# Performance work log

Hardware: AMD Instinct MI355X
Metric: run time of the kernel (lower is better)

## Reference

```python
import jax, jax.numpy as jnp
import numpy as np

B, N, D, H = 2, 2048, 1024, 16
DH = D // H  # head dim = 64


def setup_inputs() -> dict:
    key = jax.random.key(0)
    ks = jax.random.split(key, 5)
    s = 0.02  # small init so softmax is well-behaved
    x = jax.random.normal(ks[0], (B, N, D), dtype=jnp.float32)
    mask = jnp.tril(jnp.ones((N, N), dtype=jnp.int32))[None, None]  # [1,1,N,N] causal
    Wq = jax.random.normal(ks[1], (D, D), dtype=jnp.float32) * s
    Wk = jax.random.normal(ks[2], (D, D), dtype=jnp.float32) * s
    Wv = jax.random.normal(ks[3], (D, D), dtype=jnp.float32) * s
    Wp = jax.random.normal(ks[4], (D, D), dtype=jnp.float32) * s
    zb = jnp.zeros((D,), dtype=jnp.float32)
    return {"x": x, "mask": mask, "Wq": Wq, "bq": zb, "Wk": Wk, "bk": zb,
            "Wv": Wv, "bv": zb, "Wp": Wp, "bp": zb}


def reference(x, mask, Wq, bq, Wk, bk, Wv, bv, Wp, bp):
    b, n, d = x.shape
    dh = d // H
    scale = 1.0 / np.sqrt(dh).astype(np.float32)

    def split_heads(t):  # [B,N,D] -> [B,H,N,dh]
        return t.reshape(b, n, H, dh).transpose(0, 2, 1, 3)

    q = split_heads(x @ Wq + bq)
    k = split_heads(x @ Wk + bk)
    v = split_heads(x @ Wv + bv)

    scores = jnp.einsum("bhqd,bhkd->bhqk", q, k) * scale  # [B,H,N,N]
    scores = jnp.where(mask[:, :, :n, :n] == 0, -jnp.inf, scores)
    A = jax.nn.softmax(scores, axis=-1)
    # dropout layers are identity at eval / pdrop=0
    y = jnp.einsum("bhqk,bhkd->bhqd", A, v)  # [B,H,N,dh]
    y = y.transpose(0, 2, 1, 3).reshape(b, n, d)
    y = y @ Wp + bp
    return (y, A)
```

## Files before the change

kernel.cpp:

```cpp
#include <hip/hip_runtime.h>
#include <hip/hip_bf16.h>
#include <math.h>

#define B_  2
#define N_  2048
#define D_  1024
#define H_  16
#define DH_ 64
#define QT  64
#define NQT (N_/QT)

typedef __attribute__((ext_vector_type(8))) short bf16x8;
typedef __attribute__((ext_vector_type(4))) float f32x4;

#define ASYNC16(g, l) __builtin_amdgcn_global_load_lds( \
    (const __attribute__((address_space(1))) void*)(g), \
    (__attribute__((address_space(3))) void*)(l), 16, 0, 0)

__device__ __forceinline__ short f2bf(float f) {
    __hip_bfloat16 h = __float2bfloat16(f);
    return *(short*)&h;
}

__global__ __launch_bounds__(256) void cast_kernel(
    const float* __restrict__ in, short* __restrict__ out)
{
    const int i = (blockIdx.x * 256 + threadIdx.x) * 8;
    float4 a = *(const float4*)(in + i);
    float4 b = *(const float4*)(in + i + 4);
    bf16x8 o;
    o[0] = f2bf(a.x); o[1] = f2bf(a.y); o[2] = f2bf(a.z); o[3] = f2bf(a.w);
    o[4] = f2bf(b.x); o[5] = f2bf(b.y); o[6] = f2bf(b.z); o[7] = f2bf(b.w);
    *(bf16x8*)(out + i) = o;
}

__global__ __launch_bounds__(256) void tc_kernel(
    const float* __restrict__ in, short* __restrict__ out, int K, int Nc)
{
    __shared__ float t[64][65];
    const int tid = threadIdx.x;
    const int k0 = blockIdx.y * 64, n0 = blockIdx.x * 64;
    #pragma unroll
    for (int p = 0; p < 4; ++p) {
        const int r = p * 16 + (tid >> 4);
        const int c = (tid & 15) * 4;
        float4 v = *(const float4*)(in + (size_t)(k0 + r) * Nc + n0 + c);
        t[r][c] = v.x; t[r][c+1] = v.y; t[r][c+2] = v.z; t[r][c+3] = v.w;
    }
    __syncthreads();
    #pragma unroll
    for (int p = 0; p < 4; ++p) {
        const int n = p * 16 + (tid >> 4);
        const int c = (tid & 15) * 4;
        ushort4 o;
        o.x = (unsigned short)f2bf(t[c + 0][n]);
        o.y = (unsigned short)f2bf(t[c + 1][n]);
        o.z = (unsigned short)f2bf(t[c + 2][n]);
        o.w = (unsigned short)f2bf(t[c + 3][n]);
        *(ushort4*)(out + (size_t)(n0 + n) * K + k0 + c) = o;
    }
}

__global__ __launch_bounds__(256) void gemm_mfma(
    const short* __restrict__ A, const short* __restrict__ Bt,
    const float* __restrict__ bias, void* __restrict__ outv,
    int M, int Nc, int K, int mode)
{
    __shared__ short As[128 * 64];
    __shared__ short Bs[128 * 64];

    const int tid  = threadIdx.x;
    const int w    = tid >> 6;
    const int lane = tid & 63;
    const int quad = lane >> 4;
    const int col  = lane & 15;
    const int wr   = (w >> 1) * 64;
    const int wc   = (w & 1) * 64;

    const int rowBase = blockIdx.y * 128;
    const int colBase = blockIdx.x * 128;

    const int srow = tid >> 3;
    const int scol = (tid & 7) * 8;

    f32x4 acc[4][4];
    #pragma unroll
    for (int i = 0; i < 4; ++i)
        #pragma unroll
        for (int j = 0; j < 4; ++j) acc[i][j] = (f32x4){0.f, 0.f, 0.f, 0.f};

    for (int k0 = 0; k0 < K; k0 += 64) {
        __syncthreads();
        #pragma unroll
        for (int i = 0; i < 4; ++i) {
            ASYNC16(A + (size_t)(rowBase + i * 32 + srow) * K + k0 + scol,
                    As + i * 2048 + tid * 8);
            ASYNC16(Bt + (size_t)(colBase + i * 32 + srow) * K + k0 + scol,
                    Bs + i * 2048 + tid * 8);
        }
        __syncthreads();

        #pragma unroll
        for (int kk = 0; kk < 2; ++kk) {
            bf16x8 af[4], bf[4];
            #pragma unroll
            for (int mt = 0; mt < 4; ++mt)
                af[mt] = *(const bf16x8*)&As[(wr + mt * 16 + col) * 64 + kk * 32 + quad * 8];
            #pragma unroll
            for (int nt = 0; nt < 4; ++nt)
                bf[nt] = *(const bf16x8*)&Bs[(wc + nt * 16 + col) * 64 + kk * 32 + quad * 8];
            #pragma unroll
            for (int mt = 0; mt < 4; ++mt)
                #pragma unroll
                for (int nt = 0; nt < 4; ++nt)
                    acc[mt][nt] = __builtin_amdgcn_mfma_f32_16x16x32_bf16(
                        af[mt], bf[nt], acc[mt][nt], 0, 0, 0);
        }
    }

    #pragma unroll
    for (int mt = 0; mt < 4; ++mt) {
        #pragma unroll
        for (int r = 0; r < 4; ++r) {
            const int rr = rowBase + wr + mt * 16 + quad * 4 + r;
            #pragma unroll
            for (int nt = 0; nt < 4; ++nt) {
                const int cc = colBase + wc + nt * 16 + col;
                float v = acc[mt][nt][r] + bias[cc];
                if (mode == 1) {
                    ((float*)outv)[(size_t)rr * Nc + cc] = v;
                } else {
                    const int b  = rr >> 11;
                    const int n  = rr & (N_ - 1);
                    const int h  = cc >> 6;
                    const int dh = cc & 63;
                    short hv = f2bf(v);
                    if (mode == 0)
                        ((short*)outv)[(((size_t)(b * H_ + h)) * N_ + n) * DH_ + dh] = hv;
                    else
                        ((short*)outv)[(((size_t)(b * H_ + h)) * DH_ + dh) * N_ + n] = hv;
                }
            }
        }
    }
}

__global__ __launch_bounds__(256) void attn_mfma_kernel(
    const __hip_bfloat16* __restrict__ Qb, const __hip_bfloat16* __restrict__ Kb,
    const __hip_bfloat16* __restrict__ Vtb, float* __restrict__ Aout,
    short* __restrict__ Ypre)
{
    __shared__ short p_lds[4][16][72];

    const int tid  = threadIdx.x;
    const int w    = tid >> 6;
    const int lane = tid & 63;
    const int quad = lane >> 4;
    const int col  = lane & 15;

    const int bid = blockIdx.x;
    const int bh  = bid & 31;
    const int qt  = (NQT - 1) - (bid >> 5);
    const int qbase = qt * QT;
    const size_t kvbase = (size_t)bh * N_ * DH_;

    const short* Qs = (const short*)Qb + kvbase;
    const short* Ks = (const short*)Kb + kvbase;
    const short* Vs = (const short*)Vtb + kvbase;

    const short* qrow = Qs + (size_t)(qbase + w * 16 + col) * DH_ + quad * 8;
    const bf16x8 qf0 = *(const bf16x8*)(qrow);
    const bf16x8 qf1 = *(const bf16x8*)(qrow + 32);

    const int mrow_g = qbase + w * 16 + quad * 4;

    float mrun[4] = {-1e30f, -1e30f, -1e30f, -1e30f};
    float lrun[4] = {0.f, 0.f, 0.f, 0.f};

    const int njt = qt + 1;

    for (int jt = 0; jt < njt; ++jt) {
        const int jbase = jt * QT;
        f32x4 s[4];
        #pragma unroll
        for (int nt = 0; nt < 4; ++nt) {
            const short* krow = Ks + (size_t)(jbase + nt * 16 + col) * DH_ + quad * 8;
            bf16x8 k0 = *(const bf16x8*)(krow);
            bf16x8 k1 = *(const bf16x8*)(krow + 32);
            f32x4 c = {0.f, 0.f, 0.f, 0.f};
            c = __builtin_amdgcn_mfma_f32_16x16x32_bf16(qf0, k0, c, 0, 0, 0);
            c = __builtin_amdgcn_mfma_f32_16x16x32_bf16(qf1, k1, c, 0, 0, 0);
            s[nt] = c;
        }
        const bool diag = (jt == qt);
        #pragma unroll
        for (int nt = 0; nt < 4; ++nt) {
            const int n_g = jbase + nt * 16 + col;
            #pragma unroll
            for (int r = 0; r < 4; ++r) {
                float v = s[nt][r] * 0.125f;
                if (diag && (n_g > mrow_g + r)) v = -1e30f;
                s[nt][r] = v;
            }
        }
        #pragma unroll
        for (int r = 0; r < 4; ++r) {
            float tmax = fmaxf(fmaxf(s[0][r], s[1][r]), fmaxf(s[2][r], s[3][r]));
            #pragma unroll
            for (int off = 1; off < 16; off <<= 1)
                tmax = fmaxf(tmax, __shfl_xor(tmax, off));
            float mnew = fmaxf(mrun[r], tmax);
            float psum = __expf(s[0][r] - mnew) + __expf(s[1][r] - mnew)
                       + __expf(s[2][r] - mnew) + __expf(s[3][r] - mnew);
            #pragma unroll
            for (int off = 1; off < 16; off <<= 1)
                psum += __shfl_xor(psum, off);
            lrun[r] = lrun[r] * __expf(mrun[r] - mnew) + psum;
            mrun[r] = mnew;
        }
    }

    float invl[4];
    #pragma unroll
    for (int r = 0; r < 4; ++r) invl[r] = 1.0f / lrun[r];

    f32x4 yacc[4] = {{0.f,0.f,0.f,0.f},{0.f,0.f,0.f,0.f},{0.f,0.f,0.f,0.f},{0.f,0.f,0.f,0.f}};

    for (int jt = 0; jt < njt; ++jt) {
        const int jbase = jt * QT;
        f32x4 s[4];
        #pragma unroll
        for (int nt = 0; nt < 4; ++nt) {
            const short* krow = Ks + (size_t)(jbase + nt * 16 + col) * DH_ + quad * 8;
            bf16x8 k0 = *(const bf16x8*)(krow);
            bf16x8 k1 = *(const bf16x8*)(krow + 32);
            f32x4 c = {0.f, 0.f, 0.f, 0.f};
            c = __builtin_amdgcn_mfma_f32_16x16x32_bf16(qf0, k0, c, 0, 0, 0);
            c = __builtin_amdgcn_mfma_f32_16x16x32_bf16(qf1, k1, c, 0, 0, 0);
            s[nt] = c;
        }
        const bool diag = (jt == qt);
        #pragma unroll
        for (int nt = 0; nt < 4; ++nt) {
            const int n_g = jbase + nt * 16 + col;
            #pragma unroll
            for (int r = 0; r < 4; ++r) {
                float v = s[nt][r] * 0.125f;
                if (diag && (n_g > mrow_g + r)) v = -1e30f;
                float p = __expf(v - mrun[r]);
                Aout[((size_t)bh * N_ + (mrow_g + r)) * N_ + n_g] = p * invl[r];
                p_lds[w][quad * 4 + r][nt * 16 + col] = f2bf(p);
            }
        }
        bf16x8 pa0 = *(const bf16x8*)&p_lds[w][col][quad * 8];
        bf16x8 pa1 = *(const bf16x8*)&p_lds[w][col][32 + quad * 8];
        #pragma unroll
        for (int dt = 0; dt < 4; ++dt) {
            const short* vrow = Vs + (size_t)(dt * 16 + col) * N_ + jbase + quad * 8;
            bf16x8 v0 = *(const bf16x8*)(vrow);
            bf16x8 v1 = *(const bf16x8*)(vrow + 32);
            yacc[dt] = __builtin_amdgcn_mfma_f32_16x16x32_bf16(pa0, v0, yacc[dt], 0, 0, 0);
            yacc[dt] = __builtin_amdgcn_mfma_f32_16x16x32_bf16(pa1, v1, yacc[dt], 0, 0, 0);
        }
    }

    const int b = bh >> 4, h = bh & 15;
    #pragma unroll
    for (int dt = 0; dt < 4; ++dt)
        #pragma unroll
        for (int r = 0; r < 4; ++r)
            Ypre[((size_t)b * N_ + mrow_g + r) * D_ + h * DH_ + dt * 16 + col]
                = f2bf(yacc[dt][r] * invl[r]);

    float4 z; z.x = 0.f; z.y = 0.f; z.z = 0.f; z.w = 0.f;
    for (int r = 0; r < QT; ++r) {
        float4* row = (float4*)(Aout + ((size_t)bh * N_ + qbase + r) * N_);
        for (int c4 = (qt + 1) * (QT / 4) + tid; c4 < N_ / 4; c4 += 256)
            row[c4] = z;
    }
}

extern "C" void kernel_launch(void* const* d_in, const int* in_sizes, int n_in,
                              void* d_out, int out_size, void* d_ws, size_t ws_size,
                              hipStream_t stream) {
    const float* x  = (const float*)d_in[0];
    const float* Wq = (const float*)d_in[2];
    const float* bq = (const float*)d_in[3];
    const float* Wk = (const float*)d_in[4];
    const float* bk = (const float*)d_in[5];
    const float* Wv = (const float*)d_in[6];
    const float* bv = (const float*)d_in[7];
    const float* Wp = (const float*)d_in[8];
    const float* bp = (const float*)d_in[9];

    float* out_y = (float*)d_out;
    float* out_A = out_y + (size_t)B_ * N_ * D_;

    const size_t qkv = (size_t)B_ * H_ * N_ * DH_;
    const size_t wsz = (size_t)D_ * D_;
    short* Q    = (short*)d_ws;
    short* K    = Q + qkv;
    short* Vt   = K + qkv;
    short* xb   = Vt + qkv;
    short* Ypre = xb + qkv;
    short* Wqt  = Ypre + qkv;
    short* Wkt  = Wqt + wsz;
    short* Wvt  = Wkt + wsz;
    short* Wpt  = Wvt + wsz;

    const int M = B_ * N_;
    dim3 ggrid(D_ / 128, M / 128);
    dim3 tgrid(D_ / 64, D_ / 64);

    cast_kernel<<<(int)(qkv / (256 * 8)), 256, 0, stream>>>(x, xb);
    tc_kernel<<<tgrid, 256, 0, stream>>>(Wq, Wqt, D_, D_);
    tc_kernel<<<tgrid, 256, 0, stream>>>(Wk, Wkt, D_, D_);
    tc_kernel<<<tgrid, 256, 0, stream>>>(Wv, Wvt, D_, D_);
    tc_kernel<<<tgrid, 256, 0, stream>>>(Wp, Wpt, D_, D_);

    gemm_mfma<<<ggrid, 256, 0, stream>>>(xb, Wqt, bq, Q,  M, D_, D_, 0);
    gemm_mfma<<<ggrid, 256, 0, stream>>>(xb, Wkt, bk, K,  M, D_, D_, 0);
    gemm_mfma<<<ggrid, 256, 0, stream>>>(xb, Wvt, bv, Vt, M, D_, D_, 2);

    attn_mfma_kernel<<<NQT * B_ * H_, 256, 0, stream>>>(
        (const __hip_bfloat16*)Q, (const __hip_bfloat16*)K,
        (const __hip_bfloat16*)Vt, out_A, Ypre);

    gemm_mfma<<<ggrid, 256, 0, stream>>>(Ypre, Wpt, bp, out_y, M, D_, D_, 1);
}
```

Baseline: 867.3 us.

## Transpose attention score MFMA so each lane owns one query row

The attention kernel swaps the MFMA operand order so each lane holds one query row's scores across four consecutive keys. The per-row softmax statistics then need only two cross-quad shuffles instead of four-step butterflies per row, and the A matrix can be written with float4 stores instead of scattered scalar stores. The launcher also batches the four weight transposes into one grid and the three QKV projections into one GEMM launch, cutting launch count and idle tail. The row inverse-sum is staged through LDS for the Y epilogue, which relies on each warp writing and reading only its own slot.

```diff
diff --git a/kernel.cpp b/kernel.cpp
--- a/kernel.cpp
+++ b/kernel.cpp
@@ -34,17 +34,23 @@
     *(bf16x8*)(out + i) = o;
 }
 
-__global__ __launch_bounds__(256) void tc_kernel(
-    const float* __restrict__ in, short* __restrict__ out, int K, int Nc)
+__global__ __launch_bounds__(256) void tc4_kernel(
+    const float* __restrict__ Wq, const float* __restrict__ Wk,
+    const float* __restrict__ Wv, const float* __restrict__ Wp,
+    short* __restrict__ out_base)
 {
     __shared__ float t[64][65];
+    const int z = blockIdx.z;
+    const float* in = (z == 0) ? Wq : (z == 1) ? Wk : (z == 2) ? Wv : Wp;
+    short* out = out_base + (size_t)z * D_ * D_;
+
     const int tid = threadIdx.x;
     const int k0 = blockIdx.y * 64, n0 = blockIdx.x * 64;
     #pragma unroll
     for (int p = 0; p < 4; ++p) {
         const int r = p * 16 + (tid >> 4);
         const int c = (tid & 15) * 4;
-        float4 v = *(const float4*)(in + (size_t)(k0 + r) * Nc + n0 + c);
+        float4 v = *(const float4*)(in + (size_t)(k0 + r) * D_ + n0 + c);
         t[r][c] = v.x; t[r][c+1] = v.y; t[r][c+2] = v.z; t[r][c+3] = v.w;
     }
     __syncthreads();
@@ -57,18 +63,16 @@
         o.y = (unsigned short)f2bf(t[c + 1][n]);
         o.z = (unsigned short)f2bf(t[c + 2][n]);
         o.w = (unsigned short)f2bf(t[c + 3][n]);
-        *(ushort4*)(out + (size_t)(n0 + n) * K + k0 + c) = o;
-    }
-}
-
-__global__ __launch_bounds__(256) void gemm_mfma(
+        *(ushort4*)(out + (size_t)(n0 + n) * D_ + k0 + c) = o;
+    }
+}
+
+__device__ __forceinline__ void gemm_body(
     const short* __restrict__ A, const short* __restrict__ Bt,
     const float* __restrict__ bias, void* __restrict__ outv,
-    int M, int Nc, int K, int mode)
-{
-    __shared__ short As[128 * 64];
-    __shared__ short Bs[128 * 64];
-
+    int M, int Nc, int K, int mode,
+    short* As, short* Bs, int rowBase, int colBase)
+{
     const int tid  = threadIdx.x;
     const int w    = tid >> 6;
     const int lane = tid & 63;
@@ -77,9 +81,6 @@
     const int wr   = (w >> 1) * 64;
     const int wc   = (w & 1) * 64;
 
-    const int rowBase = blockIdx.y * 128;
-    const int colBase = blockIdx.x * 128;
-
     const int srow = tid >> 3;
     const int scol = (tid & 7) * 8;
 
@@ -102,19 +103,19 @@
 
         #pragma unroll
         for (int kk = 0; kk < 2; ++kk) {
-            bf16x8 af[4], bf[4];
+            bf16x8 af[4], bfr[4];
             #pragma unroll
             for (int mt = 0; mt < 4; ++mt)
                 af[mt] = *(const bf16x8*)&As[(wr + mt * 16 + col) * 64 + kk * 32 + quad * 8];
             #pragma unroll
             for (int nt = 0; nt < 4; ++nt)
-                bf[nt] = *(const bf16x8*)&Bs[(wc + nt * 16 + col) * 64 + kk * 32 + quad * 8];
+                bfr[nt] = *(const bf16x8*)&Bs[(wc + nt * 16 + col) * 64 + kk * 32 + quad * 8];
             #pragma unroll
             for (int mt = 0; mt < 4; ++mt)
                 #pragma unroll
                 for (int nt = 0; nt < 4; ++nt)
                     acc[mt][nt] = __builtin_amdgcn_mfma_f32_16x16x32_bf16(
-                        af[mt], bf[nt], acc[mt][nt], 0, 0, 0);
+                        af[mt], bfr[nt], acc[mt][nt], 0, 0, 0);
         }
     }
 
@@ -145,12 +146,39 @@
     }
 }
 
+__global__ __launch_bounds__(256) void gemm_mfma(
+    const short* __restrict__ A, const short* __restrict__ Bt,
+    const float* __restrict__ bias, void* __restrict__ outv,
+    int M, int Nc, int K, int mode)
+{
+    __shared__ short As[128 * 64];
+    __shared__ short Bs[128 * 64];
+    gemm_body(A, Bt, bias, outv, M, Nc, K, mode, As, Bs,
+              blockIdx.y * 128, blockIdx.x * 128);
+}
+
+__global__ __launch_bounds__(256) void gemm_qkv(
+    const short* __restrict__ A, const short* __restrict__ Wt3,
+    const float* __restrict__ bq, const float* __restrict__ bk,
+    const float* __restrict__ bv, short* __restrict__ Qbase, int M, int K)
+{
+    __shared__ short As[128 * 64];
+    __shared__ short Bs[128 * 64];
+    const int z = blockIdx.z;
+    const float* bias = (z == 0) ? bq : (z == 1) ? bk : bv;
+    const size_t qkv = (size_t)B_ * H_ * N_ * DH_;
+    gemm_body(A, Wt3 + (size_t)z * D_ * D_, bias,
+              Qbase + (size_t)z * qkv, M, D_, K, (z == 2) ? 2 : 0,
+              As, Bs, blockIdx.y * 128, blockIdx.x * 128);
+}
+
 __global__ __launch_bounds__(256) void attn_mfma_kernel(
     const __hip_bfloat16* __restrict__ Qb, const __hip_bfloat16* __restrict__ Kb,
     const __hip_bfloat16* __restrict__ Vtb, float* __restrict__ Aout,
     short* __restrict__ Ypre)
 {
     __shared__ short p_lds[4][16][72];
+    __shared__ float invl_sm[4][16];
 
     const int tid  = threadIdx.x;
     const int w    = tid >> 6;
@@ -172,11 +200,9 @@
     const bf16x8 qf0 = *(const bf16x8*)(qrow);
     const bf16x8 qf1 = *(const bf16x8*)(qrow + 32);
 
-    const int mrow_g = qbase + w * 16 + quad * 4;
-
-    float mrun[4] = {-1e30f, -1e30f, -1e30f, -1e30f};
-    float lrun[4] = {0.f, 0.f, 0.f, 0.f};
-
+    const int q_g = qbase + w * 16 + col;
+
+    float mrun = -1e30f, lrun = 0.f;
     const int njt = qt + 1;
 
     for (int jt = 0; jt < njt; ++jt) {
@@ -188,43 +214,43 @@
             bf16x8 k0 = *(const bf16x8*)(krow);
             bf16x8 k1 = *(const bf16x8*)(krow + 32);
             f32x4 c = {0.f, 0.f, 0.f, 0.f};
-            c = __builtin_amdgcn_mfma_f32_16x16x32_bf16(qf0, k0, c, 0, 0, 0);
-            c = __builtin_amdgcn_mfma_f32_16x16x32_bf16(qf1, k1, c, 0, 0, 0);
+            c = __builtin_amdgcn_mfma_f32_16x16x32_bf16(k0, qf0, c, 0, 0, 0);
+            c = __builtin_amdgcn_mfma_f32_16x16x32_bf16(k1, qf1, c, 0, 0, 0);
             s[nt] = c;
         }
         const bool diag = (jt == qt);
+        float tmax = -1e30f;
         #pragma unroll
         for (int nt = 0; nt < 4; ++nt) {
-            const int n_g = jbase + nt * 16 + col;
             #pragma unroll
             for (int r = 0; r < 4; ++r) {
                 float v = s[nt][r] * 0.125f;
-                if (diag && (n_g > mrow_g + r)) v = -1e30f;
+                const int n_g = jbase + nt * 16 + quad * 4 + r;
+                if (diag && (n_g > q_g)) v = -1e30f;
                 s[nt][r] = v;
+                tmax = fmaxf(tmax, v);
             }
         }
-        #pragma unroll
-        for (int r = 0; r < 4; ++r) {
-            float tmax = fmaxf(fmaxf(s[0][r], s[1][r]), fmaxf(s[2][r], s[3][r]));
-            #pragma unroll
-            for (int off = 1; off < 16; off <<= 1)
-                tmax = fmaxf(tmax, __shfl_xor(tmax, off));
-            float mnew = fmaxf(mrun[r], tmax);
-            float psum = __expf(s[0][r] - mnew) + __expf(s[1][r] - mnew)
-                       + __expf(s[2][r] - mnew) + __expf(s[3][r] - mnew);
-            #pragma unroll
-            for (int off = 1; off < 16; off <<= 1)
-                psum += __shfl_xor(psum, off);
-            lrun[r] = lrun[r] * __expf(mrun[r] - mnew) + psum;
-            mrun[r] = mnew;
-        }
-    }
-
-    float invl[4];
-    #pragma unroll
-    for (int r = 0; r < 4; ++r) invl[r] = 1.0f / lrun[r];
+        tmax = fmaxf(tmax, __shfl_xor(tmax, 16));
+        tmax = fmaxf(tmax, __shfl_xor(tmax, 32));
+        const float mnew = fmaxf(mrun, tmax);
+        float psum = 0.f;
+        #pragma unroll
+        for (int nt = 0; nt < 4; ++nt)
+            #pragma unroll
+            for (int r = 0; r < 4; ++r)
+                psum += __expf(s[nt][r] - mnew);
+        psum += __shfl_xor(psum, 16);
+        psum += __shfl_xor(psum, 32);
+        lrun = lrun * __expf(mrun - mnew) + psum;
+        mrun = mnew;
+    }
+
+    const float invl = 1.0f / lrun;
+    if (quad == 0) invl_sm[w][col] = invl;
 
     f32x4 yacc[4] = {{0.f,0.f,0.f,0.f},{0.f,0.f,0.f,0.f},{0.f,0.f,0.f,0.f},{0.f,0.f,0.f,0.f}};
+    float* Arow = Aout + ((size_t)bh * N_ + q_g) * N_;
 
     for (int jt = 0; jt < njt; ++jt) {
         const int jbase = jt * QT;
@@ -235,22 +261,37 @@
             bf16x8 k0 = *(const bf16x8*)(krow);
             bf16x8 k1 = *(const bf16x8*)(krow + 32);
             f32x4 c = {0.f, 0.f, 0.f, 0.f};
-            c = __builtin_amdgcn_mfma_f32_16x16x32_bf16(qf0, k0, c, 0, 0, 0);
-            c = __builtin_amdgcn_mfma_f32_16x16x32_bf16(qf1, k1, c, 0, 0, 0);
+            c = __builtin_amdgcn_mfma_f32_16x16x32_bf16(k0, qf0, c, 0, 0, 0);
+            c = __builtin_amdgcn_mfma_f32_16x16x32_bf16(k1, qf1, c, 0, 0, 0);
             s[nt] = c;
         }
         const bool diag = (jt == qt);
         #pragma unroll
         for (int nt = 0; nt < 4; ++nt) {
-            const int n_g = jbase + nt * 16 + col;
-            #pragma unroll
-            for (int r = 0; r < 4; ++r) {
-                float v = s[nt][r] * 0.125f;
-                if (diag && (n_g > mrow_g + r)) v = -1e30f;
-                float p = __expf(v - mrun[r]);
-                Aout[((size_t)bh * N_ + (mrow_g + r)) * N_ + n_g] = p * invl[r];
-                p_lds[w][quad * 4 + r][nt * 16 + col] = f2bf(p);
+            float p0, p1, p2, p3;
+            {
+                float v0 = s[nt][0] * 0.125f;
+                float v1 = s[nt][1] * 0.125f;
+                float v2 = s[nt][2] * 0.125f;
+                float v3 = s[nt][3] * 0.125f;
+                const int nb = jbase + nt * 16 + quad * 4;
+                if (diag) {
+                    if (nb + 0 > q_g) v0 = -1e30f;
+                    if (nb + 1 > q_g) v1 = -1e30f;
+                    if (nb + 2 > q_g) v2 = -1e30f;
+                    if (nb + 3 > q_g) v3 = -1e30f;
+                }
+                p0 = __expf(v0 - mrun); p1 = __expf(v1 - mrun);
+                p2 = __expf(v2 - mrun); p3 = __expf(v3 - mrun);
             }
+            float4 a;
+            a.x = p0 * invl; a.y = p1 * invl; a.z = p2 * invl; a.w = p3 * invl;
+            *(float4*)(Arow + jbase + nt * 16 + quad * 4) = a;
+            const unsigned int lo = (unsigned int)(unsigned short)f2bf(p0)
+                                  | ((unsigned int)(unsigned short)f2bf(p1) << 16);
+            const unsigned int hi = (unsigned int)(unsigned short)f2bf(p2)
+                                  | ((unsigned int)(unsigned short)f2bf(p3) << 16);
+            *(uint2*)&p_lds[w][col][nt * 16 + quad * 4] = make_uint2(lo, hi);
         }
         bf16x8 pa0 = *(const bf16x8*)&p_lds[w][col][quad * 8];
         bf16x8 pa1 = *(const bf16x8*)&p_lds[w][col][32 + quad * 8];
@@ -265,12 +306,13 @@
     }
 
     const int b = bh >> 4, h = bh & 15;
+    const int mrow_g = qbase + w * 16 + quad * 4;
     #pragma unroll
     for (int dt = 0; dt < 4; ++dt)
         #pragma unroll
         for (int r = 0; r < 4; ++r)
             Ypre[((size_t)b * N_ + mrow_g + r) * D_ + h * DH_ + dt * 16 + col]
-                = f2bf(yacc[dt][r] * invl[r]);
+                = f2bf(yacc[dt][r] * invl_sm[w][quad * 4 + r]);
 
     float4 z; z.x = 0.f; z.y = 0.f; z.z = 0.f; z.w = 0.f;
     for (int r = 0; r < QT; ++r) {
@@ -304,27 +346,20 @@
     short* xb   = Vt + qkv;
     short* Ypre = xb + qkv;
     short* Wqt  = Ypre + qkv;
-    short* Wkt  = Wqt + wsz;
-    short* Wvt  = Wkt + wsz;
-    short* Wpt  = Wvt + wsz;
+    short* Wpt  = Wqt + 3 * wsz;
 
     const int M = B_ * N_;
-    dim3 ggrid(D_ / 128, M / 128);
-    dim3 tgrid(D_ / 64, D_ / 64);
 
     cast_kernel<<<(int)(qkv / (256 * 8)), 256, 0, stream>>>(x, xb);
-    tc_kernel<<<tgrid, 256, 0, stream>>>(Wq, Wqt, D_, D_);
-    tc_kernel<<<tgrid, 256, 0, stream>>>(Wk, Wkt, D_, D_);
-    tc_kernel<<<tgrid, 256, 0, stream>>>(Wv, Wvt, D_, D_);
-    tc_kernel<<<tgrid, 256, 0, stream>>>(Wp, Wpt, D_, D_);
-
-    gemm_mfma<<<ggrid, 256, 0, stream>>>(xb, Wqt, bq, Q,  M, D_, D_, 0);
-    gemm_mfma<<<ggrid, 256, 0, stream>>>(xb, Wkt, bk, K,  M, D_, D_, 0);
-    gemm_mfma<<<ggrid, 256, 0, stream>>>(xb, Wvt, bv, Vt, M, D_, D_, 2);
+    tc4_kernel<<<dim3(D_ / 64, D_ / 64, 4), 256, 0, stream>>>(Wq, Wk, Wv, Wp, Wqt);
+
+    gemm_qkv<<<dim3(D_ / 128, M / 128, 3), 256, 0, stream>>>(
+        xb, Wqt, bq, bk, bv, Q, M, D_);
 
     attn_mfma_kernel<<<NQT * B_ * H_, 256, 0, stream>>>(
         (const __hip_bfloat16*)Q, (const __hip_bfloat16*)K,
         (const __hip_bfloat16*)Vt, out_A, Ypre);
 
-    gemm_mfma<<<ggrid, 256, 0, stream>>>(Ypre, Wpt, bp, out_y, M, D_, D_, 1);
-}
+    gemm_mfma<<<dim3(D_ / 128, M / 128), 256, 0, stream>>>(
+        Ypre, Wpt, bp, out_y, M, D_, D_, 1);
+}
```

Result: faster. 835.8 us (-3.6%).
